# Performance work log

Hardware: AMD Instinct MI355X
Metric: run time of the kernel (lower is better)

The kernel has to match this reference:

```python
import jax, jax.numpy as jnp
import numpy as np

EXPERTS, IN_DIM, OUT_DIM, BATCH = 8, 1024, 1024, 16384

def setup_inputs() -> dict:
    key = jax.random.key(0)
    k1, k2, k3, k4 = jax.random.split(key, 4)
    bound = np.sqrt(6.0 / (IN_DIM * OUT_DIM)).astype(np.float32)
    bbound = np.sqrt(6.0 / (1 * OUT_DIM)).astype(np.float32)
    return {
        "x": jax.random.normal(k1, (BATCH, IN_DIM), dtype=jnp.float32),
        "weights": jax.random.uniform(k2, (BATCH, EXPERTS), dtype=jnp.float32),
        "W": jax.random.uniform(k3, (EXPERTS, IN_DIM, OUT_DIM), jnp.float32, -bound, bound),
        "b": jax.random.uniform(k4, (EXPERTS, 1, OUT_DIM), jnp.float32, -bbound, bbound),
    }

def reference(x, weights, W, b):
    # y[b,o] = sum_e weights[b,e] * (x[b,:] @ W[e] + b[e])
    # Fused triple einsum avoids materializing the [B,E,O] intermediate.
    y = jnp.einsum("be,bi,eio->bo", weights, x, W)
    y = y + jnp.einsum("be,eo->bo", weights, b[:, 0, :])
    return y
```

## Files before the change

### kernel.cpp

```cpp
#include <hip/hip_runtime.h>
#include <hip/hip_bf16.h>
#include <stdint.h>

#define BATCH   16384
#define EXPERTS 8
#define IN_DIM  1024
#define OUT_DIM 1024

typedef unsigned short u16;
typedef short  bf16x8 __attribute__((ext_vector_type(8)));
typedef float  f32x4  __attribute__((ext_vector_type(4)));

__device__ __forceinline__ u16 f2bf(float f) {
  uint32_t u = __float_as_uint(f);
  u += 0x7fffu + ((u >> 16) & 1u);
  return (u16)(u >> 16);
}

#define GLDS16(g, l)                                                      \
  __builtin_amdgcn_global_load_lds(                                       \
      (const __attribute__((address_space(1))) void*)(g),                 \
      (__attribute__((address_space(3))) void*)(l), 16, 0, 0)

#define MFMA_BF16 __builtin_amdgcn_mfma_f32_16x16x32_bf16

__global__ void cvt_x(const float* __restrict__ x, u16* __restrict__ xb) {
  size_t i = ((size_t)blockIdx.x * 256 + threadIdx.x) * 4;
  float4 v = *reinterpret_cast<const float4*>(x + i);
  ushort4 o;
  o.x = f2bf(v.x); o.y = f2bf(v.y); o.z = f2bf(v.z); o.w = f2bf(v.w);
  *reinterpret_cast<ushort4*>(xb + i) = o;
}

__global__ void cvt_w(const float* __restrict__ W, u16* __restrict__ wbt) {
  __shared__ u16 t[64][72];
  const int e  = blockIdx.z;
  const int i0 = blockIdx.x * 64;
  const int o0 = blockIdx.y * 64;
  const int tid = threadIdx.x;
  const int c  = (tid & 15) * 4;
  const int r_ = tid >> 4;
  const float* src = W + ((size_t)e << 20);
#pragma unroll
  for (int p = 0; p < 4; ++p) {
    int r = r_ + p * 16;
    float4 v = *reinterpret_cast<const float4*>(src + (size_t)(i0 + r) * 1024 + o0 + c);
    t[r][c + 0] = f2bf(v.x); t[r][c + 1] = f2bf(v.y);
    t[r][c + 2] = f2bf(v.z); t[r][c + 3] = f2bf(v.w);
  }
  __syncthreads();
  u16* dst = wbt + ((size_t)e << 20);
#pragma unroll
  for (int p = 0; p < 4; ++p) {
    int orow = r_ + p * 16;
    ushort4 u;
    u.x = t[c + 0][orow]; u.y = t[c + 1][orow];
    u.z = t[c + 2][orow]; u.w = t[c + 3][orow];
    *reinterpret_cast<ushort4*>(dst + (size_t)(o0 + orow) * 1024 + i0 + c) = u;
  }
}

__global__ __launch_bounds__(512, 2)
void zgemm(const u16* __restrict__ xb, const u16* __restrict__ wbt,
           const float* __restrict__ wts, const float* __restrict__ bias,
           float* __restrict__ y) {
  __shared__ u16 sm[69632];
  char* smb = (char*)sm;
  float* rl = (float*)(sm + 65536);

  const int tid = threadIdx.x;
  const int l   = tid & 63;
  const int w   = tid >> 6;
  const int wm  = w >> 2;
  const int wn  = w & 3;
  const int x8  = blockIdx.x & 7;
  const int jj  = blockIdx.x >> 3;
  const int n0  = (x8 >> 1) * 256;
  const int b0  = (((x8 & 1) << 5) + jj) << 8;

#pragma unroll
  for (int i = 0; i < 4; ++i) {
    const int flat = tid + i * 512;
    const int e = flat & 7, r = flat >> 3;
    const float* wr = wts + (size_t)(b0 + r) * EXPERTS;
    float we = fmaxf(wr[e], 1e-20f);
    float rr = (e < 7) ? we / fmaxf(wr[e + 1], 1e-20f) : we;
    rl[e * 256 + r] = rr;
  }

  const int rb    = (w << 3) + (l >> 3);
  const int chunk = ((l & 7) ^ (l >> 3)) << 3;
  const u16* pAg = xb  + (size_t)(b0 + rb) * IN_DIM + chunk;
  const u16* pBg = wbt + (size_t)(n0 + rb) * 1024 + chunk;

  const int l15  = l & 15;
  const int kb0  = (((l >> 4) << 4)) ^ ((l & 7) << 4);
  const int arow = (wm * 128 + l15) * 128;
  const int brow = (wn * 64 + l15) * 128;
  const int wlo  = (wm << 9) + ((l >> 4) << 4);

  f32x4 acc[8][4];
#pragma unroll
  for (int m = 0; m < 8; ++m)
#pragma unroll
    for (int n = 0; n < 4; ++n) acc[m][n] = (f32x4){0.f, 0.f, 0.f, 0.f};

#define STG_A(q, dstE, ev_kv)                                              \
  GLDS16(pAg + (size_t)((q) * 64) * 1024 + (ev_kv),                        \
         sm + (dstE) + (q) * 4096 + (w << 9))
#define STG_B(q, dstE, off)                                                \
  GLDS16(pBg + (off) + (size_t)((q) * 64) * 1024,                          \
         sm + (dstE) + (q) * 4096 + (w << 9))

  STG_A(0, 0, 0); STG_A(1, 0, 0); STG_A(2, 0, 0); STG_A(3, 0, 0);
  STG_B(0, 32768, 0); STG_B(1, 32768, 0); STG_B(2, 32768, 0); STG_B(3, 32768, 0);
  asm volatile("s_waitcnt vmcnt(0)" ::: "memory");
  asm volatile("s_waitcnt lgkmcnt(0)" ::: "memory");
  __builtin_amdgcn_s_barrier();

#define CLUSTER(AV, BV, MB)                                                \
  __builtin_amdgcn_s_barrier();                                            \
  asm volatile("s_waitcnt lgkmcnt(0)" ::: "memory");                       \
  __builtin_amdgcn_sched_barrier(0);                                       \
  __builtin_amdgcn_s_setprio(1);                                           \
  _Pragma("unroll")                                                        \
  for (int m = 0; m < 4; ++m)                                              \
    _Pragma("unroll")                                                      \
    for (int n = 0; n < 4; ++n)                                            \
      acc[(MB) + m][n] = MFMA_BF16(AV[m], BV[n], acc[(MB) + m][n], 0, 0, 0); \
  __builtin_amdgcn_s_setprio(0);

#pragma unroll 1
  for (int t = 0; t < 128; ++t) {
    const int tn  = (t + 1) & 127;
    const int e1  = tn >> 4, k1 = tn & 15;
    const int ArB = (t & 1) << 15;
    const int AwE = ((t + 1) & 1) << 14;
    const int BrB = 65536 + ((t & 1) << 15);
    const int BwE = 32768 + (((t + 1) & 1) << 14);
    const size_t aoffg = (size_t)k1 * 64;
    const size_t boffg = (size_t)e1 * 1048576 + (size_t)k1 * 64;

    bf16x8 a[4], b[4];

#pragma unroll
    for (int m = 0; m < 4; ++m)
      a[m] = *(const bf16x8*)(smb + ArB + arow + m * 2048 + kb0);
#pragma unroll
    for (int n = 0; n < 4; ++n)
      b[n] = *(const bf16x8*)(smb + BrB + brow + n * 2048 + kb0);
    STG_A(0, AwE, aoffg); STG_A(1, AwE, aoffg);
    STG_A(2, AwE, aoffg); STG_A(3, AwE, aoffg);
    STG_B(0, BwE, boffg); STG_B(1, BwE, boffg);
    STG_B(2, BwE, boffg); STG_B(3, BwE, boffg);
    CLUSTER(a, b, 0)
    __builtin_amdgcn_s_barrier();

    bf16x8 a2[4];
#pragma unroll
    for (int m = 0; m < 4; ++m)
      a2[m] = *(const bf16x8*)(smb + ArB + arow + (m + 4) * 2048 + kb0);
    CLUSTER(a2, b, 4)
    __builtin_amdgcn_s_barrier();

    bf16x8 b2[4];
#pragma unroll
    for (int m = 0; m < 4; ++m)
      a[m] = *(const bf16x8*)(smb + ArB + arow + m * 2048 + (kb0 ^ 64));
#pragma unroll
    for (int n = 0; n < 4; ++n)
      b2[n] = *(const bf16x8*)(smb + BrB + brow + n * 2048 + (kb0 ^ 64));
    CLUSTER(a, b2, 0)
    __builtin_amdgcn_s_barrier();

#pragma unroll
    for (int m = 0; m < 4; ++m)
      a2[m] = *(const bf16x8*)(smb + ArB + arow + (m + 4) * 2048 + (kb0 ^ 64));
    CLUSTER(a2, b2, 4)
    asm volatile("s_waitcnt vmcnt(0)" ::: "memory");
    __builtin_amdgcn_s_barrier();

    if ((t & 15) == 15 && t != 127) {
      const int e = t >> 4;
#pragma unroll
      for (int m = 0; m < 8; ++m) {
        const f32x4 rv = *(const f32x4*)(smb + 131072 + e * 1024 + wlo + m * 64);
#pragma unroll
        for (int n = 0; n < 4; ++n) acc[m][n] *= rv;
      }
    }
  }
  asm volatile("s_waitcnt vmcnt(0)" ::: "memory");

  float bv[4][8];
#pragma unroll
  for (int n = 0; n < 4; ++n) {
    const int c = n0 + wn * 64 + n * 16 + l15;
#pragma unroll
    for (int ee = 0; ee < 8; ++ee) bv[n][ee] = bias[ee * OUT_DIM + c];
  }
#pragma unroll
  for (int m = 0; m < 8; ++m) {
    const f32x4 rv7 = *(const f32x4*)(smb + 131072 + 7 * 1024 + wlo + m * 64);
    const int r0 = b0 + wm * 128 + m * 16 + ((l >> 4) << 2);
#pragma unroll
    for (int j = 0; j < 4; ++j) {
      const float* wr = wts + (size_t)(r0 + j) * EXPERTS;
      float w8[8];
#pragma unroll
      for (int ee = 0; ee < 8; ++ee) w8[ee] = wr[ee];
#pragma unroll
      for (int n = 0; n < 4; ++n) {
        const int c = n0 + wn * 64 + n * 16 + l15;
        float v = acc[m][n][j] * rv7[j];
#pragma unroll
        for (int ee = 0; ee < 8; ++ee) v += w8[ee] * bv[n][ee];
        y[(size_t)(r0 + j) * OUT_DIM + c] = v;
      }
    }
  }
}

extern "C" void kernel_launch(void* const* d_in, const int* in_sizes, int n_in,
                              void* d_out, int out_size, void* d_ws, size_t ws_size,
                              hipStream_t stream) {
  const float* x    = (const float*)d_in[0];
  const float* wts  = (const float*)d_in[1];
  const float* W    = (const float*)d_in[2];
  const float* bias = (const float*)d_in[3];
  float* y = (float*)d_out;

  const size_t xb_elems = (size_t)BATCH * IN_DIM;
  const size_t wb_elems = (size_t)EXPERTS * IN_DIM * OUT_DIM;
  if (ws_size < (xb_elems + wb_elems) * sizeof(u16)) return;
  u16* xb  = (u16*)d_ws;
  u16* wbt = xb + xb_elems;

  cvt_x<<<(BATCH * IN_DIM) / (4 * 256), 256, 0, stream>>>(x, xb);
  cvt_w<<<dim3(IN_DIM / 64, OUT_DIM / 64, EXPERTS), 256, 0, stream>>>(W, wbt);
  zgemm<<<dim3(256), 512, 0, stream>>>(xb, wbt, wts, bias, y);
}
```

Before: 287.9 us.

## Software-pipeline LDS fragment reads with MFMA clusters and drop intra-iteration barriers

Restructures the inner k-loop so LDS fragment reads for the next MFMA cluster are issued before the current cluster runs. Partial lgkmcnt waits now gate each cluster instead of full waits. The seven per-iteration s_barriers between clusters are removed, leaving one barrier per iteration after the vmcnt wait. This aims to hide LDS latency behind MFMA work and cut barrier stalls, but it uses more vector registers for the extra fragment buffers, which may lower occupancy under the 512x2 launch bounds. The lgkmcnt counts must match the issued loads, and the global_load_lds traffic also interacts with these counters.

```diff
diff --git a/kernel.cpp b/kernel.cpp
--- a/kernel.cpp
+++ b/kernel.cpp
@@ -23,6 +23,8 @@
       (__attribute__((address_space(3))) void*)(l), 16, 0, 0)
 
 #define MFMA_BF16 __builtin_amdgcn_mfma_f32_16x16x32_bf16
+#define SB0 __builtin_amdgcn_sched_barrier(0)
+#define LGKM(N) asm volatile("s_waitcnt lgkmcnt(" #N ")" ::: "memory")
 
 __global__ void cvt_x(const float* __restrict__ x, u16* __restrict__ xb) {
   size_t i = ((size_t)blockIdx.x * 256 + threadIdx.x) * 4;
@@ -115,13 +117,10 @@
   STG_A(0, 0, 0); STG_A(1, 0, 0); STG_A(2, 0, 0); STG_A(3, 0, 0);
   STG_B(0, 32768, 0); STG_B(1, 32768, 0); STG_B(2, 32768, 0); STG_B(3, 32768, 0);
   asm volatile("s_waitcnt vmcnt(0)" ::: "memory");
-  asm volatile("s_waitcnt lgkmcnt(0)" ::: "memory");
+  LGKM(0);
   __builtin_amdgcn_s_barrier();
 
-#define CLUSTER(AV, BV, MB)                                                \
-  __builtin_amdgcn_s_barrier();                                            \
-  asm volatile("s_waitcnt lgkmcnt(0)" ::: "memory");                       \
-  __builtin_amdgcn_sched_barrier(0);                                       \
+#define MM(AV, BV, MB)                                                     \
   __builtin_amdgcn_s_setprio(1);                                           \
   _Pragma("unroll")                                                        \
   for (int m = 0; m < 4; ++m)                                              \
@@ -141,42 +140,43 @@
     const size_t aoffg = (size_t)k1 * 64;
     const size_t boffg = (size_t)e1 * 1048576 + (size_t)k1 * 64;
 
-    bf16x8 a[4], b[4];
-
-#pragma unroll
-    for (int m = 0; m < 4; ++m)
-      a[m] = *(const bf16x8*)(smb + ArB + arow + m * 2048 + kb0);
+    bf16x8 a0[4], b0v[4], a1[4], a2v[4], b1v[4], a3[4];
+
+#pragma unroll
+    for (int m = 0; m < 4; ++m)
+      a0[m] = *(const bf16x8*)(smb + ArB + arow + m * 2048 + kb0);
 #pragma unroll
     for (int n = 0; n < 4; ++n)
-      b[n] = *(const bf16x8*)(smb + BrB + brow + n * 2048 + kb0);
+      b0v[n] = *(const bf16x8*)(smb + BrB + brow + n * 2048 + kb0);
+#pragma unroll
+    for (int m = 0; m < 4; ++m)
+      a1[m] = *(const bf16x8*)(smb + ArB + arow + (m + 4) * 2048 + kb0);
     STG_A(0, AwE, aoffg); STG_A(1, AwE, aoffg);
     STG_A(2, AwE, aoffg); STG_A(3, AwE, aoffg);
     STG_B(0, BwE, boffg); STG_B(1, BwE, boffg);
     STG_B(2, BwE, boffg); STG_B(3, BwE, boffg);
-    CLUSTER(a, b, 0)
-    __builtin_amdgcn_s_barrier();
-
-    bf16x8 a2[4];
-#pragma unroll
-    for (int m = 0; m < 4; ++m)
-      a2[m] = *(const bf16x8*)(smb + ArB + arow + (m + 4) * 2048 + kb0);
-    CLUSTER(a2, b, 4)
-    __builtin_amdgcn_s_barrier();
-
-    bf16x8 b2[4];
-#pragma unroll
-    for (int m = 0; m < 4; ++m)
-      a[m] = *(const bf16x8*)(smb + ArB + arow + m * 2048 + (kb0 ^ 64));
+
+    LGKM(4); SB0;
+#pragma unroll
+    for (int m = 0; m < 4; ++m)
+      a2v[m] = *(const bf16x8*)(smb + ArB + arow + m * 2048 + (kb0 ^ 64));
 #pragma unroll
     for (int n = 0; n < 4; ++n)
-      b2[n] = *(const bf16x8*)(smb + BrB + brow + n * 2048 + (kb0 ^ 64));
-    CLUSTER(a, b2, 0)
-    __builtin_amdgcn_s_barrier();
-
-#pragma unroll
-    for (int m = 0; m < 4; ++m)
-      a2[m] = *(const bf16x8*)(smb + ArB + arow + (m + 4) * 2048 + (kb0 ^ 64));
-    CLUSTER(a2, b2, 4)
+      b1v[n] = *(const bf16x8*)(smb + BrB + brow + n * 2048 + (kb0 ^ 64));
+    MM(a0, b0v, 0)
+
+    LGKM(8); SB0;
+#pragma unroll
+    for (int m = 0; m < 4; ++m)
+      a3[m] = *(const bf16x8*)(smb + ArB + arow + (m + 4) * 2048 + (kb0 ^ 64));
+    MM(a1, b0v, 4)
+
+    LGKM(4); SB0;
+    MM(a2v, b1v, 0)
+
+    LGKM(0); SB0;
+    MM(a3, b1v, 4)
+
     asm volatile("s_waitcnt vmcnt(0)" ::: "memory");
     __builtin_amdgcn_s_barrier();
 
@@ -188,6 +188,7 @@
 #pragma unroll
         for (int n = 0; n < 4; ++n) acc[m][n] *= rv;
       }
+      LGKM(0); SB0;
     }
   }
   asm volatile("s_waitcnt vmcnt(0)" ::: "memory");
```

After: 259.7 us. -9.8%, faster.
